# Optimization experiments

Hardware: AMD Instinct MI355X
Metric: run time of the kernel (lower is better)

The kernel has to match this reference:

```python
import jax, jax.numpy as jnp
import numpy as np

DIM = 1024
NUM_HEADS = 16
HD = DIM // NUM_HEADS  # 64
ROPE_DIM = 64
ROPE_BASE = 10000.0


def setup_inputs() -> dict:
    key = jax.random.key(0)
    ks = jax.random.split(key, 5)
    B, N = 2, 2048
    s = 0.02
    return {
        "x": jax.random.normal(ks[0], (B, N, DIM), dtype=jnp.float32),
        "qkv_w": jax.random.normal(ks[1], (3 * DIM, DIM), dtype=jnp.float32) * s,
        "qkv_b": jax.random.normal(ks[2], (3 * DIM,), dtype=jnp.float32) * s,
        "proj_w": jax.random.normal(ks[3], (DIM, DIM), dtype=jnp.float32) * s,
        "proj_b": jax.random.normal(ks[4], (DIM,), dtype=jnp.float32) * s,
    }


def _apply_rope(t):
    # t: [B, H, N, D] with D even; interleaved (even, odd) pair rotation
    D = t.shape[-1]
    N = t.shape[2]
    pos = jnp.arange(N, dtype=t.dtype)
    inv = 1.0 / (ROPE_BASE ** (jnp.arange(0, D, 2, dtype=t.dtype) / D))
    freqs = pos[:, None] * inv[None, :]          # [N, D/2]
    cos = jnp.cos(freqs)[None, None]             # [1,1,N,D/2]
    sin = jnp.sin(freqs)[None, None]
    e = t[..., 0::2]
    o = t[..., 1::2]
    eo = e * cos - o * sin
    oo = e * sin + o * cos
    return jnp.stack([eo, oo], axis=-1).reshape(t.shape)


def reference(x, qkv_w, qkv_b, proj_w, proj_b):
    B, N, C = x.shape
    H, D = NUM_HEADS, HD
    scale = D ** -0.5
    qkv = x @ qkv_w.T + qkv_b                     # [B,N,3C]
    qkv = qkv.reshape(B, N, 3, H, D).transpose(2, 0, 3, 1, 4)  # [3,B,H,N,D]
    q, k, v = qkv[0], qkv[1], qkv[2]
    # RoPE on first ROPE_DIM dims of each head (here ROPE_DIM == HD)
    q = jnp.concatenate([_apply_rope(q[..., :ROPE_DIM]), q[..., ROPE_DIM:]], axis=-1)
    k = jnp.concatenate([_apply_rope(k[..., :ROPE_DIM]), k[..., ROPE_DIM:]], axis=-1)
    attn = jnp.einsum('bhnd,bhmd->bhnm', q, k) * scale
    attn = jax.nn.softmax(attn, axis=-1)
    out = jnp.einsum('bhnm,bhmd->bhnd', attn, v)  # [B,H,N,D]
    out = out.transpose(0, 2, 1, 3).reshape(B, N, C)
    return out @ proj_w.T + proj_b
```

## Files before the change

### kernel.cpp

```cpp
#include <hip/hip_runtime.h>
#include <hip/hip_bf16.h>
#include <stdint.h>

#define DIM   1024
#define NH    16
#define HDIM  64
#define SEQ   2048
#define BATCH 2
#define BHN   32
#define MTOK  4096
#define SC2   0.18033688f

using u16 = unsigned short;
using u32 = unsigned int;
typedef __attribute__((ext_vector_type(8))) short short8;
typedef __attribute__((ext_vector_type(4))) float f32x4;
typedef __attribute__((ext_vector_type(16))) float f32x16;

__device__ __forceinline__ u16 f2bf(float f) {
  __hip_bfloat16 h = __float2bfloat16(f);
  return *reinterpret_cast<u16*>(&h);
}
__device__ __forceinline__ u32 pk2(float lo, float hi) {
  return (u32)f2bf(lo) | ((u32)f2bf(hi) << 16);
}
__device__ __forceinline__ u32 cvtpk(float lo, float hi) {
  u32 r;
  asm("v_cvt_pk_bf16_f32 %0, %1, %2" : "=v"(r) : "v"(lo), "v"(hi));
  return r;
}
__device__ __forceinline__ float vexp2(float x) {
  float r;
  asm("v_exp_f32 %0, %1" : "=v"(r) : "v"(x));
  return r;
}

__device__ __forceinline__ void gload16(const void* g, void* lds) {
  __builtin_amdgcn_global_load_lds(
      (const __attribute__((address_space(1))) u32*)g,
      (__attribute__((address_space(3))) u32*)lds, 16, 0, 0);
}

#define PREP_A 1048576
#define PREP_B 1835008
#define PREP_C 2097152
#define PREP_E 2162688
__global__ void k_prep(const float4* __restrict__ x, const float4* __restrict__ qw,
                       const float4* __restrict__ pw, ushort4* __restrict__ xb,
                       ushort4* __restrict__ qwb, ushort4* __restrict__ pwb,
                       float2* __restrict__ tab) {
  int i = blockIdx.x * blockDim.x + threadIdx.x;
  if (i < PREP_A) {
    float4 v = x[i];
    xb[i] = make_ushort4(f2bf(v.x), f2bf(v.y), f2bf(v.z), f2bf(v.w));
  } else if (i < PREP_B) {
    int j = i - PREP_A;
    float4 v = qw[j];
    qwb[j] = make_ushort4(f2bf(v.x), f2bf(v.y), f2bf(v.z), f2bf(v.w));
  } else if (i < PREP_C) {
    int j = i - PREP_B;
    float4 v = pw[j];
    pwb[j] = make_ushort4(f2bf(v.x), f2bf(v.y), f2bf(v.z), f2bf(v.w));
  } else if (i < PREP_E) {
    int j = i - PREP_C;
    int n = j >> 5, f = j & 31;
    float inv = powf(10000.f, -(2.f * f) / 64.f);
    float s, c;
    sincosf((float)n * inv, &s, &c);
    tab[j] = make_float2(c, s);
  }
}

template <int EPI>
__global__ __launch_bounds__(256, 2) void k_gemm(
    const u16* __restrict__ A, const u16* __restrict__ Bt,
    const float* __restrict__ bias, int K,
    float* __restrict__ out_f, u16* __restrict__ qb, u16* __restrict__ kb,
    u16* __restrict__ vtb, const float2* __restrict__ tab) {
  __shared__ u16 As[128 * 64];
  __shared__ u16 Bs[128 * 64];
  const int tid = threadIdx.x;
  const int wid = tid >> 6, lane = tid & 63;
  const int lq = lane & 15, g = lane >> 4;
  const int wr = wid >> 1, wc = wid & 1;
  const int brow = blockIdx.y * 128;
  const int bcol = blockIdx.x * 128;
  f32x4 acc[4][4] = {};
  const u16* Ab = A + (size_t)brow * K;
  const u16* Bb = Bt + (size_t)bcol * K;

  for (int k0 = 0; k0 < K; k0 += 64) {
#pragma unroll
    for (int t = 0; t < 4; t++) {
      int rl = wid * 32 + t * 8 + (lane >> 3);
      int cs = (lane & 7) ^ (rl & 7);
      gload16(Ab + (size_t)rl * K + k0 + cs * 8, &As[(wid * 32 + t * 8) * 64]);
      gload16(Bb + (size_t)rl * K + k0 + cs * 8, &Bs[(wid * 32 + t * 8) * 64]);
    }
    __syncthreads();
#pragma unroll
    for (int kc = 0; kc < 2; kc++) {
      short8 af[4], bfr[4];
#pragma unroll
      for (int mt = 0; mt < 4; mt++) {
        int r = wr * 64 + mt * 16 + lq;
        af[mt] = *reinterpret_cast<const short8*>(&As[r * 64 + (((kc * 4 + g) ^ (r & 7)) * 8)]);
      }
#pragma unroll
      for (int nt = 0; nt < 4; nt++) {
        int r = wc * 64 + nt * 16 + lq;
        bfr[nt] = *reinterpret_cast<const short8*>(&Bs[r * 64 + (((kc * 4 + g) ^ (r & 7)) * 8)]);
      }
#pragma unroll
      for (int mt = 0; mt < 4; mt++)
#pragma unroll
        for (int nt = 0; nt < 4; nt++)
          acc[mt][nt] = __builtin_amdgcn_mfma_f32_16x16x32_bf16(af[mt], bfr[nt], acc[mt][nt], 0, 0, 0);
    }
    __syncthreads();
  }

#pragma unroll
  for (int mt = 0; mt < 4; mt++) {
    int row0 = brow + wr * 64 + mt * 16 + g * 4;
#pragma unroll
    for (int nt = 0; nt < 4; nt++) {
      int col = bcol + wc * 64 + nt * 16 + lq;
      float bv = bias[col];
      float v[4];
#pragma unroll
      for (int r = 0; r < 4; r++) v[r] = acc[mt][nt][r] + bv;
      if (EPI == 0) {
#pragma unroll
        for (int r = 0; r < 4; r++) out_f[(size_t)(row0 + r) * DIM + col] = v[r];
      } else {
        int which = col >> 10, hd = col & 1023, hdh = hd >> 6, d = hd & 63;
        int bb = row0 >> 11, n0 = row0 & 2047;
        int bh = bb * NH + hdh;
        if (which == 2) {
          uint2 pv = make_uint2(pk2(v[0], v[1]), pk2(v[2], v[3]));
          size_t idx = ((((size_t)bh * 32 + (n0 >> 6)) * 8 + ((n0 >> 3) & 7)) * 64 + d) * 8 + (n0 & 7);
          *reinterpret_cast<uint2*>(&vtb[idx]) = pv;
        } else {
#pragma unroll
          for (int r = 0; r < 4; r++) {
            int n = n0 + r;
            float p = __shfl_xor(v[r], 1);
            float2 cs = tab[n * 32 + (d >> 1)];
            float vv = (d & 1) ? fmaf(p, cs.y, v[r] * cs.x)
                               : fmaf(-p, cs.y, v[r] * cs.x);
            if (which == 0) {
              qb[((size_t)bh * SEQ + n) * HDIM + d] = f2bf(vv * SC2);
            } else {
              size_t idx = ((((size_t)bh * 32 + (n >> 6)) * 8 + (d >> 3)) * 64 + (n & 63)) * 8 + (d & 7);
              kb[idx] = f2bf(vv);
            }
          }
        }
      }
    }
  }
}

__global__ __launch_bounds__(256) void k_attn(
    const u16* __restrict__ qg, const u16* __restrict__ kg,
    const u16* __restrict__ vg, u16* __restrict__ aout) {
  const int tid = threadIdx.x;
  const int wid = tid >> 6, lane = tid & 63;
  const int l31 = lane & 31, h = lane >> 5;

  const int bid = blockIdx.x;
  const int xcd = bid & 7, slot = bid >> 3;
  const int bh = xcd * 4 + (slot >> 4);
  const int qt = slot & 15;
  const int b = bh >> 4, hh = bh & 15;
  const int q0 = qt * 128 + wid * 32;

  const u16* kb0 = kg + (size_t)bh * SEQ * HDIM + h * 512 + l31 * 8;
  const u16* vb0 = vg + (size_t)bh * SEQ * HDIM + h * 512 + l31 * 8;

  const u16* qrow = qg + ((size_t)bh * SEQ + q0 + l31) * HDIM;
  short8 qf[4];
#pragma unroll
  for (int c = 0; c < 4; c++)
    qf[c] = *reinterpret_cast<const short8*>(qrow + c * 16 + h * 8);

  short8 ones;
#pragma unroll
  for (int i = 0; i < 8; i++) ones[i] = (short)0x3F80;

  short8 kf[8], vf[8];
#pragma unroll
  for (int c = 0; c < 4; c++) {
    kf[2 * c]     = *reinterpret_cast<const short8*>(kb0 + c * 1024);
    kf[2 * c + 1] = *reinterpret_cast<const short8*>(kb0 + c * 1024 + 256);
    vf[2 * c]     = *reinterpret_cast<const short8*>(vb0 + c * 1024);
    vf[2 * c + 1] = *reinterpret_cast<const short8*>(vb0 + c * 1024 + 256);
  }

  f32x16 oA = {}, oB = {}, ls = {};

  const int NT = SEQ / 64;
  for (int t = 0; t < NT; ++t) {
    f32x16 s0 = {}, s1 = {};
    __builtin_amdgcn_s_setprio(1);
#pragma unroll
    for (int c = 0; c < 4; c++) {
      s0 = __builtin_amdgcn_mfma_f32_32x32x16_bf16(kf[2 * c],     qf[c], s0, 0, 0, 0);
      s1 = __builtin_amdgcn_mfma_f32_32x32x16_bf16(kf[2 * c + 1], qf[c], s1, 0, 0, 0);
    }
    __builtin_amdgcn_s_setprio(0);

    if (t + 1 < NT) {
      const u16* kn = kb0 + (size_t)(t + 1) * 4096;
#pragma unroll
      for (int c = 0; c < 4; c++) {
        kf[2 * c]     = *reinterpret_cast<const short8*>(kn + c * 1024);
        kf[2 * c + 1] = *reinterpret_cast<const short8*>(kn + c * 1024 + 256);
      }
    }

#pragma unroll
    for (int r = 0; r < 16; r++) s0[r] = vexp2(s0[r]);
#pragma unroll
    for (int r = 0; r < 16; r++) s1[r] = vexp2(s1[r]);

    short8 pf[4];
    {
      union { u32 u[4]; short8 v; } pp;
      u32 a0, a1, b0, b1;
      a0 = cvtpk(s0[0], s0[1]);  a1 = cvtpk(s0[2], s0[3]);
      b0 = cvtpk(s0[4], s0[5]);  b1 = cvtpk(s0[6], s0[7]);
      { auto r0 = __builtin_amdgcn_permlane32_swap(a0, b0, false, false);
        auto r1 = __builtin_amdgcn_permlane32_swap(a1, b1, false, false);
        pp.u[0] = r0[0]; pp.u[1] = r1[0]; pp.u[2] = r0[1]; pp.u[3] = r1[1]; pf[0] = pp.v; }
      a0 = cvtpk(s0[8], s0[9]);   a1 = cvtpk(s0[10], s0[11]);
      b0 = cvtpk(s0[12], s0[13]); b1 = cvtpk(s0[14], s0[15]);
      { auto r0 = __builtin_amdgcn_permlane32_swap(a0, b0, false, false);
        auto r1 = __builtin_amdgcn_permlane32_swap(a1, b1, false, false);
        pp.u[0] = r0[0]; pp.u[1] = r1[0]; pp.u[2] = r0[1]; pp.u[3] = r1[1]; pf[1] = pp.v; }
      a0 = cvtpk(s1[0], s1[1]);  a1 = cvtpk(s1[2], s1[3]);
      b0 = cvtpk(s1[4], s1[5]);  b1 = cvtpk(s1[6], s1[7]);
      { auto r0 = __builtin_amdgcn_permlane32_swap(a0, b0, false, false);
        auto r1 = __builtin_amdgcn_permlane32_swap(a1, b1, false, false);
        pp.u[0] = r0[0]; pp.u[1] = r1[0]; pp.u[2] = r0[1]; pp.u[3] = r1[1]; pf[2] = pp.v; }
      a0 = cvtpk(s1[8], s1[9]);   a1 = cvtpk(s1[10], s1[11]);
      b0 = cvtpk(s1[12], s1[13]); b1 = cvtpk(s1[14], s1[15]);
      { auto r0 = __builtin_amdgcn_permlane32_swap(a0, b0, false, false);
        auto r1 = __builtin_amdgcn_permlane32_swap(a1, b1, false, false);
        pp.u[0] = r0[0]; pp.u[1] = r1[0]; pp.u[2] = r0[1]; pp.u[3] = r1[1]; pf[3] = pp.v; }
    }

    __builtin_amdgcn_s_setprio(1);
#pragma unroll
    for (int c = 0; c < 4; c++) {
      oA = __builtin_amdgcn_mfma_f32_32x32x16_bf16(vf[2 * c],     pf[c], oA, 0, 0, 0);
      oB = __builtin_amdgcn_mfma_f32_32x32x16_bf16(vf[2 * c + 1], pf[c], oB, 0, 0, 0);
      ls = __builtin_amdgcn_mfma_f32_32x32x16_bf16(ones,          pf[c], ls, 0, 0, 0);
    }
    __builtin_amdgcn_s_setprio(0);

    if (t + 1 < NT) {
      const u16* vn = vb0 + (size_t)(t + 1) * 4096;
#pragma unroll
      for (int c = 0; c < 4; c++) {
        vf[2 * c]     = *reinterpret_cast<const short8*>(vn + c * 1024);
        vf[2 * c + 1] = *reinterpret_cast<const short8*>(vn + c * 1024 + 256);
      }
    }
  }

  float invl = 1.0f / ls[0];
  int n = q0 + l31;
  u16* op = aout + ((size_t)(b * SEQ + n)) * DIM + hh * HDIM;
#pragma unroll
  for (int g = 0; g < 4; g++) {
    u32 w0 = pk2(oA[4 * g] * invl, oA[4 * g + 1] * invl);
    u32 w1 = pk2(oA[4 * g + 2] * invl, oA[4 * g + 3] * invl);
    *reinterpret_cast<uint2*>(op + 8 * g + 4 * h) = make_uint2(w0, w1);
    u32 x0 = pk2(oB[4 * g] * invl, oB[4 * g + 1] * invl);
    u32 x1 = pk2(oB[4 * g + 2] * invl, oB[4 * g + 3] * invl);
    *reinterpret_cast<uint2*>(op + 32 + 8 * g + 4 * h) = make_uint2(x0, x1);
  }
}

extern "C" void kernel_launch(void* const* d_in, const int* in_sizes, int n_in,
                              void* d_out, int out_size, void* d_ws, size_t ws_size,
                              hipStream_t stream) {
  (void)in_sizes; (void)n_in; (void)out_size; (void)ws_size;
  const float* x      = (const float*)d_in[0];
  const float* qkv_w  = (const float*)d_in[1];
  const float* qkv_b  = (const float*)d_in[2];
  const float* proj_w = (const float*)d_in[3];
  const float* proj_b = (const float*)d_in[4];
  float* out = (float*)d_out;

  char* w = (char*)d_ws;
  u16* xb     = (u16*)w;  w += (size_t)MTOK * DIM * 2;
  u16* wqkvb  = (u16*)w;  w += (size_t)3 * DIM * DIM * 2;
  u16* wprojb = (u16*)w;  w += (size_t)DIM * DIM * 2;
  u16* qb     = (u16*)w;  w += (size_t)BHN * SEQ * HDIM * 2;
  u16* kb     = (u16*)w;  w += (size_t)BHN * SEQ * HDIM * 2;
  u16* vtb    = (u16*)w;  w += (size_t)BHN * SEQ * HDIM * 2;
  u16* aout   = (u16*)w;  w += (size_t)MTOK * DIM * 2;
  float2* tab = (float2*)w;

  k_prep<<<(PREP_E + 255) / 256, 256, 0, stream>>>(
      (const float4*)x, (const float4*)qkv_w, (const float4*)proj_w,
      (ushort4*)xb, (ushort4*)wqkvb, (ushort4*)wprojb, tab);

  k_gemm<1><<<dim3(3 * DIM / 128, MTOK / 128), 256, 0, stream>>>(
      xb, wqkvb, qkv_b, DIM, nullptr, qb, kb, vtb, tab);

  k_attn<<<512, 256, 0, stream>>>(qb, kb, vtb, aout);

  k_gemm<0><<<dim3(DIM / 128, MTOK / 128), 256, 0, stream>>>(
      aout, wprojb, proj_b, DIM, out, nullptr, nullptr, nullptr, nullptr);
}
```

Measured before the change: 135.2 us.

## Software-pipeline attention loop so QK of next tile overlaps PV of previous

Restructures the attention inner loop into a software pipeline: the QK^T MFMAs for tile t+1 are issued before the PV MFMAs for tile t, with V double-buffered in registers (vfA/vfB) and the loop unrolled by two. The goal is to hide the exp/pack latency and global-load latency behind independent matrix work. It uses more registers for the second V buffer, which may lower occupancy or cause spills.

```diff
diff --git a/kernel.cpp b/kernel.cpp
--- a/kernel.cpp
+++ b/kernel.cpp
@@ -189,20 +189,36 @@
 #pragma unroll
   for (int i = 0; i < 8; i++) ones[i] = (short)0x3F80;
 
-  short8 kf[8], vf[8];
-#pragma unroll
-  for (int c = 0; c < 4; c++) {
-    kf[2 * c]     = *reinterpret_cast<const short8*>(kb0 + c * 1024);
-    kf[2 * c + 1] = *reinterpret_cast<const short8*>(kb0 + c * 1024 + 256);
-    vf[2 * c]     = *reinterpret_cast<const short8*>(vb0 + c * 1024);
-    vf[2 * c + 1] = *reinterpret_cast<const short8*>(vb0 + c * 1024 + 256);
-  }
-
+  short8 kf[8], vfA[8], vfB[8], pfp[4];
   f32x16 oA = {}, oB = {}, ls = {};
-
-  const int NT = SEQ / 64;
-  for (int t = 0; t < NT; ++t) {
-    f32x16 s0 = {}, s1 = {};
+  f32x16 s0, s1;
+
+  auto loadK = [&](int t) {
+    const u16* kn = kb0 + (size_t)t * 4096;
+#pragma unroll
+    for (int c = 0; c < 4; c++) {
+      kf[2 * c]     = *reinterpret_cast<const short8*>(kn + c * 1024);
+      kf[2 * c + 1] = *reinterpret_cast<const short8*>(kn + c * 1024 + 256);
+    }
+  };
+  auto loadVA = [&](int t) {
+    const u16* vn = vb0 + (size_t)t * 4096;
+#pragma unroll
+    for (int c = 0; c < 4; c++) {
+      vfA[2 * c]     = *reinterpret_cast<const short8*>(vn + c * 1024);
+      vfA[2 * c + 1] = *reinterpret_cast<const short8*>(vn + c * 1024 + 256);
+    }
+  };
+  auto loadVB = [&](int t) {
+    const u16* vn = vb0 + (size_t)t * 4096;
+#pragma unroll
+    for (int c = 0; c < 4; c++) {
+      vfB[2 * c]     = *reinterpret_cast<const short8*>(vn + c * 1024);
+      vfB[2 * c + 1] = *reinterpret_cast<const short8*>(vn + c * 1024 + 256);
+    }
+  };
+  auto qk = [&]() {
+    s0 = (f32x16){}; s1 = (f32x16){};
     __builtin_amdgcn_s_setprio(1);
 #pragma unroll
     for (int c = 0; c < 4; c++) {
@@ -210,65 +226,80 @@
       s1 = __builtin_amdgcn_mfma_f32_32x32x16_bf16(kf[2 * c + 1], qf[c], s1, 0, 0, 0);
     }
     __builtin_amdgcn_s_setprio(0);
-
-    if (t + 1 < NT) {
-      const u16* kn = kb0 + (size_t)(t + 1) * 4096;
-#pragma unroll
-      for (int c = 0; c < 4; c++) {
-        kf[2 * c]     = *reinterpret_cast<const short8*>(kn + c * 1024);
-        kf[2 * c + 1] = *reinterpret_cast<const short8*>(kn + c * 1024 + 256);
-      }
-    }
-
+  };
+  auto pvA = [&]() {
+    __builtin_amdgcn_s_setprio(1);
+#pragma unroll
+    for (int c = 0; c < 4; c++) {
+      oA = __builtin_amdgcn_mfma_f32_32x32x16_bf16(vfA[2 * c],     pfp[c], oA, 0, 0, 0);
+      oB = __builtin_amdgcn_mfma_f32_32x32x16_bf16(vfA[2 * c + 1], pfp[c], oB, 0, 0, 0);
+      ls = __builtin_amdgcn_mfma_f32_32x32x16_bf16(ones,           pfp[c], ls, 0, 0, 0);
+    }
+    __builtin_amdgcn_s_setprio(0);
+  };
+  auto pvB = [&]() {
+    __builtin_amdgcn_s_setprio(1);
+#pragma unroll
+    for (int c = 0; c < 4; c++) {
+      oA = __builtin_amdgcn_mfma_f32_32x32x16_bf16(vfB[2 * c],     pfp[c], oA, 0, 0, 0);
+      oB = __builtin_amdgcn_mfma_f32_32x32x16_bf16(vfB[2 * c + 1], pfp[c], oB, 0, 0, 0);
+      ls = __builtin_amdgcn_mfma_f32_32x32x16_bf16(ones,           pfp[c], ls, 0, 0, 0);
+    }
+    __builtin_amdgcn_s_setprio(0);
+  };
+  auto exppack = [&]() {
 #pragma unroll
     for (int r = 0; r < 16; r++) s0[r] = vexp2(s0[r]);
 #pragma unroll
     for (int r = 0; r < 16; r++) s1[r] = vexp2(s1[r]);
-
-    short8 pf[4];
-    {
-      union { u32 u[4]; short8 v; } pp;
-      u32 a0, a1, b0, b1;
-      a0 = cvtpk(s0[0], s0[1]);  a1 = cvtpk(s0[2], s0[3]);
-      b0 = cvtpk(s0[4], s0[5]);  b1 = cvtpk(s0[6], s0[7]);
-      { auto r0 = __builtin_amdgcn_permlane32_swap(a0, b0, false, false);
-        auto r1 = __builtin_amdgcn_permlane32_swap(a1, b1, false, false);
-        pp.u[0] = r0[0]; pp.u[1] = r1[0]; pp.u[2] = r0[1]; pp.u[3] = r1[1]; pf[0] = pp.v; }
-      a0 = cvtpk(s0[8], s0[9]);   a1 = cvtpk(s0[10], s0[11]);
-      b0 = cvtpk(s0[12], s0[13]); b1 = cvtpk(s0[14], s0[15]);
-      { auto r0 = __builtin_amdgcn_permlane32_swap(a0, b0, false, false);
-        auto r1 = __builtin_amdgcn_permlane32_swap(a1, b1, false, false);
-        pp.u[0] = r0[0]; pp.u[1] = r1[0]; pp.u[2] = r0[1]; pp.u[3] = r1[1]; pf[1] = pp.v; }
-      a0 = cvtpk(s1[0], s1[1]);  a1 = cvtpk(s1[2], s1[3]);
-      b0 = cvtpk(s1[4], s1[5]);  b1 = cvtpk(s1[6], s1[7]);
-      { auto r0 = __builtin_amdgcn_permlane32_swap(a0, b0, false, false);
-        auto r1 = __builtin_amdgcn_permlane32_swap(a1, b1, false, false);
-        pp.u[0] = r0[0]; pp.u[1] = r1[0]; pp.u[2] = r0[1]; pp.u[3] = r1[1]; pf[2] = pp.v; }
-      a0 = cvtpk(s1[8], s1[9]);   a1 = cvtpk(s1[10], s1[11]);
-      b0 = cvtpk(s1[12], s1[13]); b1 = cvtpk(s1[14], s1[15]);
-      { auto r0 = __builtin_amdgcn_permlane32_swap(a0, b0, false, false);
-        auto r1 = __builtin_amdgcn_permlane32_swap(a1, b1, false, false);
-        pp.u[0] = r0[0]; pp.u[1] = r1[0]; pp.u[2] = r0[1]; pp.u[3] = r1[1]; pf[3] = pp.v; }
-    }
-
-    __builtin_amdgcn_s_setprio(1);
-#pragma unroll
-    for (int c = 0; c < 4; c++) {
-      oA = __builtin_amdgcn_mfma_f32_32x32x16_bf16(vf[2 * c],     pf[c], oA, 0, 0, 0);
-      oB = __builtin_amdgcn_mfma_f32_32x32x16_bf16(vf[2 * c + 1], pf[c], oB, 0, 0, 0);
-      ls = __builtin_amdgcn_mfma_f32_32x32x16_bf16(ones,          pf[c], ls, 0, 0, 0);
-    }
-    __builtin_amdgcn_s_setprio(0);
-
-    if (t + 1 < NT) {
-      const u16* vn = vb0 + (size_t)(t + 1) * 4096;
-#pragma unroll
-      for (int c = 0; c < 4; c++) {
-        vf[2 * c]     = *reinterpret_cast<const short8*>(vn + c * 1024);
-        vf[2 * c + 1] = *reinterpret_cast<const short8*>(vn + c * 1024 + 256);
-      }
-    }
-  }
+    union { u32 u[4]; short8 v; } pp;
+    u32 a0, a1, b0, b1;
+    a0 = cvtpk(s0[0], s0[1]);  a1 = cvtpk(s0[2], s0[3]);
+    b0 = cvtpk(s0[4], s0[5]);  b1 = cvtpk(s0[6], s0[7]);
+    { auto r0 = __builtin_amdgcn_permlane32_swap(a0, b0, false, false);
+      auto r1 = __builtin_amdgcn_permlane32_swap(a1, b1, false, false);
+      pp.u[0] = r0[0]; pp.u[1] = r1[0]; pp.u[2] = r0[1]; pp.u[3] = r1[1]; pfp[0] = pp.v; }
+    a0 = cvtpk(s0[8], s0[9]);   a1 = cvtpk(s0[10], s0[11]);
+    b0 = cvtpk(s0[12], s0[13]); b1 = cvtpk(s0[14], s0[15]);
+    { auto r0 = __builtin_amdgcn_permlane32_swap(a0, b0, false, false);
+      auto r1 = __builtin_amdgcn_permlane32_swap(a1, b1, false, false);
+      pp.u[0] = r0[0]; pp.u[1] = r1[0]; pp.u[2] = r0[1]; pp.u[3] = r1[1]; pfp[1] = pp.v; }
+    a0 = cvtpk(s1[0], s1[1]);  a1 = cvtpk(s1[2], s1[3]);
+    b0 = cvtpk(s1[4], s1[5]);  b1 = cvtpk(s1[6], s1[7]);
+    { auto r0 = __builtin_amdgcn_permlane32_swap(a0, b0, false, false);
+      auto r1 = __builtin_amdgcn_permlane32_swap(a1, b1, false, false);
+      pp.u[0] = r0[0]; pp.u[1] = r1[0]; pp.u[2] = r0[1]; pp.u[3] = r1[1]; pfp[2] = pp.v; }
+    a0 = cvtpk(s1[8], s1[9]);   a1 = cvtpk(s1[10], s1[11]);
+    b0 = cvtpk(s1[12], s1[13]); b1 = cvtpk(s1[14], s1[15]);
+    { auto r0 = __builtin_amdgcn_permlane32_swap(a0, b0, false, false);
+      auto r1 = __builtin_amdgcn_permlane32_swap(a1, b1, false, false);
+      pp.u[0] = r0[0]; pp.u[1] = r1[0]; pp.u[2] = r0[1]; pp.u[3] = r1[1]; pfp[3] = pp.v; }
+  };
+
+  loadK(0); loadVA(0);
+  qk();
+  loadK(1); loadVB(1);
+  exppack();
+
+#pragma unroll 1
+  for (int i = 0; i < 15; i++) {
+    const int t1 = 2 * i + 1;
+    qk();
+    loadK(t1 + 1);
+    pvA();
+    loadVA(t1 + 1);
+    exppack();
+    qk();
+    loadK(t1 + 2);
+    pvB();
+    loadVB(t1 + 2);
+    exppack();
+  }
+
+  qk();
+  pvA();
+  exppack();
+  pvB();
 
   float invl = 1.0f / ls[0];
   int n = q0 + l31;
```

New measurement: 129.2 us. -4.5%, faster.

## Software-pipeline attention loop to overlap next QK MFMAs with current softmax-PV

Applied to the files above, without the earlier changes.

Restructures the attention inner loop into a two-stage software pipeline with double-buffered score accumulators. The QK^T MFMAs for the next key tile are interleaved, chunk by chunk, with the exp2, bf16 pack and PV MFMAs of the current tile. K and V loads for later tiles are issued per chunk. The aim is to hide exp and permute latency behind matrix-core work and keep the MFMA pipe busy. The cost is higher register pressure from the extra score buffers, which could reduce occupancy or cause spills.

```diff
diff --git a/kernel.cpp b/kernel.cpp
--- a/kernel.cpp
+++ b/kernel.cpp
@@ -190,85 +190,93 @@
   for (int i = 0; i < 8; i++) ones[i] = (short)0x3F80;
 
   short8 kf[8], vf[8];
-#pragma unroll
-  for (int c = 0; c < 4; c++) {
-    kf[2 * c]     = *reinterpret_cast<const short8*>(kb0 + c * 1024);
-    kf[2 * c + 1] = *reinterpret_cast<const short8*>(kb0 + c * 1024 + 256);
-    vf[2 * c]     = *reinterpret_cast<const short8*>(vb0 + c * 1024);
-    vf[2 * c + 1] = *reinterpret_cast<const short8*>(vb0 + c * 1024 + 256);
-  }
-
+  f32x16 sA0, sA1, sB0, sB1;
   f32x16 oA = {}, oB = {}, ls = {};
 
-  const int NT = SEQ / 64;
-  for (int t = 0; t < NT; ++t) {
-    f32x16 s0 = {}, s1 = {};
-    __builtin_amdgcn_s_setprio(1);
+  auto loadKfull = [&](int t) {
+    const u16* kn = kb0 + (size_t)t * 4096;
 #pragma unroll
     for (int c = 0; c < 4; c++) {
-      s0 = __builtin_amdgcn_mfma_f32_32x32x16_bf16(kf[2 * c],     qf[c], s0, 0, 0, 0);
-      s1 = __builtin_amdgcn_mfma_f32_32x32x16_bf16(kf[2 * c + 1], qf[c], s1, 0, 0, 0);
-    }
-    __builtin_amdgcn_s_setprio(0);
-
-    if (t + 1 < NT) {
-      const u16* kn = kb0 + (size_t)(t + 1) * 4096;
-#pragma unroll
-      for (int c = 0; c < 4; c++) {
-        kf[2 * c]     = *reinterpret_cast<const short8*>(kn + c * 1024);
-        kf[2 * c + 1] = *reinterpret_cast<const short8*>(kn + c * 1024 + 256);
-      }
-    }
-
-#pragma unroll
-    for (int r = 0; r < 16; r++) s0[r] = vexp2(s0[r]);
-#pragma unroll
-    for (int r = 0; r < 16; r++) s1[r] = vexp2(s1[r]);
-
-    short8 pf[4];
-    {
+      kf[2 * c]     = *reinterpret_cast<const short8*>(kn + c * 1024);
+      kf[2 * c + 1] = *reinterpret_cast<const short8*>(kn + c * 1024 + 256);
+    }
+  };
+  auto loadVfull = [&](int t) {
+    const u16* vn = vb0 + (size_t)t * 4096;
+#pragma unroll
+    for (int c = 0; c < 4; c++) {
+      vf[2 * c]     = *reinterpret_cast<const short8*>(vn + c * 1024);
+      vf[2 * c + 1] = *reinterpret_cast<const short8*>(vn + c * 1024 + 256);
+    }
+  };
+
+  auto step = [&](f32x16& sc0, f32x16& sc1, f32x16& sn0, f32x16& sn1,
+                  const u16* knxt, const u16* vnxt, bool doQK, bool doK) {
+#pragma unroll
+    for (int c = 0; c < 4; c++) {
+      f32x16& sv = (c < 2) ? sc0 : sc1;
+      const int e0 = (c & 1) * 8;
+      float e[8];
+#pragma unroll
+      for (int j = 0; j < 8; j++) e[j] = vexp2(sv[e0 + j]);
+      u32 a0 = cvtpk(e[0], e[1]), a1 = cvtpk(e[2], e[3]);
+      u32 b0 = cvtpk(e[4], e[5]), b1 = cvtpk(e[6], e[7]);
+      auto r0 = __builtin_amdgcn_permlane32_swap(a0, b0, false, false);
+      auto r1 = __builtin_amdgcn_permlane32_swap(a1, b1, false, false);
       union { u32 u[4]; short8 v; } pp;
-      u32 a0, a1, b0, b1;
-      a0 = cvtpk(s0[0], s0[1]);  a1 = cvtpk(s0[2], s0[3]);
-      b0 = cvtpk(s0[4], s0[5]);  b1 = cvtpk(s0[6], s0[7]);
-      { auto r0 = __builtin_amdgcn_permlane32_swap(a0, b0, false, false);
-        auto r1 = __builtin_amdgcn_permlane32_swap(a1, b1, false, false);
-        pp.u[0] = r0[0]; pp.u[1] = r1[0]; pp.u[2] = r0[1]; pp.u[3] = r1[1]; pf[0] = pp.v; }
-      a0 = cvtpk(s0[8], s0[9]);   a1 = cvtpk(s0[10], s0[11]);
-      b0 = cvtpk(s0[12], s0[13]); b1 = cvtpk(s0[14], s0[15]);
-      { auto r0 = __builtin_amdgcn_permlane32_swap(a0, b0, false, false);
-        auto r1 = __builtin_amdgcn_permlane32_swap(a1, b1, false, false);
-        pp.u[0] = r0[0]; pp.u[1] = r1[0]; pp.u[2] = r0[1]; pp.u[3] = r1[1]; pf[1] = pp.v; }
-      a0 = cvtpk(s1[0], s1[1]);  a1 = cvtpk(s1[2], s1[3]);
-      b0 = cvtpk(s1[4], s1[5]);  b1 = cvtpk(s1[6], s1[7]);
-      { auto r0 = __builtin_amdgcn_permlane32_swap(a0, b0, false, false);
-        auto r1 = __builtin_amdgcn_permlane32_swap(a1, b1, false, false);
-        pp.u[0] = r0[0]; pp.u[1] = r1[0]; pp.u[2] = r0[1]; pp.u[3] = r1[1]; pf[2] = pp.v; }
-      a0 = cvtpk(s1[8], s1[9]);   a1 = cvtpk(s1[10], s1[11]);
-      b0 = cvtpk(s1[12], s1[13]); b1 = cvtpk(s1[14], s1[15]);
-      { auto r0 = __builtin_amdgcn_permlane32_swap(a0, b0, false, false);
-        auto r1 = __builtin_amdgcn_permlane32_swap(a1, b1, false, false);
-        pp.u[0] = r0[0]; pp.u[1] = r1[0]; pp.u[2] = r0[1]; pp.u[3] = r1[1]; pf[3] = pp.v; }
-    }
-
-    __builtin_amdgcn_s_setprio(1);
+      pp.u[0] = r0[0]; pp.u[1] = r1[0]; pp.u[2] = r0[1]; pp.u[3] = r1[1];
+      short8 pf = pp.v;
+
+      __builtin_amdgcn_s_setprio(1);
+      oA = __builtin_amdgcn_mfma_f32_32x32x16_bf16(vf[2 * c],     pf, oA, 0, 0, 0);
+      oB = __builtin_amdgcn_mfma_f32_32x32x16_bf16(vf[2 * c + 1], pf, oB, 0, 0, 0);
+      ls = __builtin_amdgcn_mfma_f32_32x32x16_bf16(ones,          pf, ls, 0, 0, 0);
+      if (doQK) {
+        if (c == 0) {
+          f32x16 z = {};
+          sn0 = __builtin_amdgcn_mfma_f32_32x32x16_bf16(kf[0], qf[0], z, 0, 0, 0);
+          sn1 = __builtin_amdgcn_mfma_f32_32x32x16_bf16(kf[1], qf[0], z, 0, 0, 0);
+        } else {
+          sn0 = __builtin_amdgcn_mfma_f32_32x32x16_bf16(kf[2 * c],     qf[c], sn0, 0, 0, 0);
+          sn1 = __builtin_amdgcn_mfma_f32_32x32x16_bf16(kf[2 * c + 1], qf[c], sn1, 0, 0, 0);
+        }
+      }
+      __builtin_amdgcn_s_setprio(0);
+
+      if (doK) {
+        kf[2 * c]     = *reinterpret_cast<const short8*>(knxt + c * 1024);
+        kf[2 * c + 1] = *reinterpret_cast<const short8*>(knxt + c * 1024 + 256);
+      }
+      vf[2 * c]     = *reinterpret_cast<const short8*>(vnxt + c * 1024);
+      vf[2 * c + 1] = *reinterpret_cast<const short8*>(vnxt + c * 1024 + 256);
+    }
+  };
+
+  loadKfull(0);
+  loadVfull(0);
+  {
+    f32x16 z = {};
+    sA0 = z; sA1 = z;
 #pragma unroll
     for (int c = 0; c < 4; c++) {
-      oA = __builtin_amdgcn_mfma_f32_32x32x16_bf16(vf[2 * c],     pf[c], oA, 0, 0, 0);
-      oB = __builtin_amdgcn_mfma_f32_32x32x16_bf16(vf[2 * c + 1], pf[c], oB, 0, 0, 0);
-      ls = __builtin_amdgcn_mfma_f32_32x32x16_bf16(ones,          pf[c], ls, 0, 0, 0);
-    }
-    __builtin_amdgcn_s_setprio(0);
-
-    if (t + 1 < NT) {
-      const u16* vn = vb0 + (size_t)(t + 1) * 4096;
-#pragma unroll
-      for (int c = 0; c < 4; c++) {
-        vf[2 * c]     = *reinterpret_cast<const short8*>(vn + c * 1024);
-        vf[2 * c + 1] = *reinterpret_cast<const short8*>(vn + c * 1024 + 256);
-      }
-    }
-  }
+      sA0 = __builtin_amdgcn_mfma_f32_32x32x16_bf16(kf[2 * c],     qf[c], sA0, 0, 0, 0);
+      sA1 = __builtin_amdgcn_mfma_f32_32x32x16_bf16(kf[2 * c + 1], qf[c], sA1, 0, 0, 0);
+    }
+  }
+  loadKfull(1);
+
+#pragma unroll 1
+  for (int i = 0; i < 15; i++) {
+    const u16* kA = kb0 + (size_t)(2 * i + 2) * 4096;
+    const u16* vA = vb0 + (size_t)(2 * i + 1) * 4096;
+    step(sA0, sA1, sB0, sB1, kA, vA, true, true);
+    const u16* kB = kb0 + (size_t)(2 * i + 3) * 4096;
+    const u16* vB = vb0 + (size_t)(2 * i + 2) * 4096;
+    step(sB0, sB1, sA0, sA1, kB, vB, true, true);
+  }
+  const u16* v31 = vb0 + (size_t)31 * 4096;
+  step(sA0, sA1, sB0, sB1, kb0, v31, true, false);
+  step(sB0, sB1, sA0, sA1, kb0, v31, false, false);
 
   float invl = 1.0f / ls[0];
   int n = q0 + l31;
```

New measurement: 126.7 us. 6.3% less time.
